# Kernel tuning notes

Hardware: AMD Instinct MI355X
Metric: run time of the kernel (lower is better)

Reference implementation:

```python
import jax, jax.numpy as jnp
import numpy as np

N_NODES = 100000
N_EDGES = 1600000
N_OBS, N_MID, N_ACT = 32, 64, 8


def setup_inputs() -> dict:
    key = jax.random.key(0)
    k1, k2, k3, k4, k5, k6 = jax.random.split(key, 6)
    x = jax.random.normal(k1, (N_NODES, N_OBS), dtype=jnp.float32)
    edge_index = jax.random.randint(k2, (2, N_EDGES), 0, N_NODES, dtype=jnp.int64)
    W1 = jax.random.normal(k3, (N_OBS, N_MID), dtype=jnp.float32) / np.sqrt(N_OBS)
    b1 = jax.random.normal(k4, (N_MID,), dtype=jnp.float32) * 0.01
    W2 = jax.random.normal(k5, (N_MID, N_ACT), dtype=jnp.float32) / np.sqrt(N_MID)
    b2 = jax.random.normal(k6, (N_ACT,), dtype=jnp.float32) * 0.01
    return {"x": x, "edge_index": edge_index, "W1": W1, "b1": b1, "W2": W2, "b2": b2}


def reference(x, edge_index, W1, b1, W2, b2):
    N = x.shape[0]
    # PyG GCNConv: add self-loops, symmetric deg^{-1/2} normalization,
    # linear transform before propagation, bias after aggregation.
    loops = jnp.arange(N, dtype=edge_index.dtype)
    src = jnp.concatenate([edge_index[0], loops])  # message sources (x_j)
    dst = jnp.concatenate([edge_index[1], loops])  # aggregation targets
    deg = jax.ops.segment_sum(jnp.ones_like(dst, dtype=x.dtype), dst, num_segments=N)
    dinv = jnp.where(deg > 0, jax.lax.rsqrt(deg), jnp.zeros_like(deg))
    norm = dinv[src] * dinv[dst]  # [E+N]
    h = x @ W1  # [N, n_mid]
    agg = jax.ops.segment_sum(h[src] * norm[:, None], dst, num_segments=N) + b1
    return jnp.tanh(agg) @ W2 + b2  # [N, n_action]
```

## Files before the change

kernel.cpp:

```cpp
#include <hip/hip_runtime.h>
#include <hip/hip_fp16.h>
#include <math.h>


#define NOBS 32
#define NMID 64
#define NACT 8
#define BSH 7
#define BNODES 128
#define CAP 4096
#define ARENA_B 16384
#define SPLIT_E 4096
#define NPW 4

__device__ __forceinline__ bool edges_i64(const int* ei) {
    return (ei[1] | ei[3] | ei[5] | ei[7]) == 0;
}

__device__ __forceinline__ float fast_tanh(float x) {
    float t = __expf(2.f * x);
    return 1.f - 2.f * __builtin_amdgcn_rcpf(1.f + t);
}

__device__ __forceinline__ float rl(float v, int lane) {
    return __int_as_float(__builtin_amdgcn_readlane(__float_as_int(v), lane));
}

__global__ __launch_bounds__(256) void k_split(
        const int* __restrict__ ei, int* __restrict__ gcnt,
        unsigned int* __restrict__ arena, long long e, int nbuckets) {
    __shared__ int sbuf[SPLIT_E];
    __shared__ int offs[1024];
    __shared__ int cur[1024];
    __shared__ int tsum[256];
    const int tid = threadIdx.x;
    int eb[16];
    int bk[16];

    for (int b = tid; b < 1024; b += 256) cur[b] = 0;
    __syncthreads();

    const long long base = (long long)blockIdx.x * SPLIT_E;
    const bool i64 = edges_i64(ei);
    const long long* e64 = (const long long*)ei;
#pragma unroll
    for (int j = 0; j < 8; ++j) {
        const int kk = j * 512 + tid * 2;
        const long long ge = base + kk;
        const bool v0 = ge < e, v1 = ge + 1 < e;
        int s0 = 0, d0 = 0, s1 = 0, d1 = 0;
        if (v1) {
            if (i64) {
                ulonglong2 sp = *(const ulonglong2*)(e64 + ge);
                ulonglong2 dp = *(const ulonglong2*)(e64 + e + ge);
                s0 = (int)sp.x; s1 = (int)sp.y; d0 = (int)dp.x; d1 = (int)dp.y;
            } else {
                int2 sp = *(const int2*)(ei + ge);
                int2 dp = *(const int2*)(ei + e + ge);
                s0 = sp.x; s1 = sp.y; d0 = dp.x; d1 = dp.y;
            }
        } else if (v0) {
            if (i64) { s0 = (int)e64[ge]; d0 = (int)e64[e + ge]; }
            else     { s0 = ei[ge];       d0 = ei[e + ge]; }
        }
        eb[2 * j]     = s0 | ((d0 & (BNODES - 1)) << 20);
        bk[2 * j]     = v0 ? (d0 >> BSH) : -1;
        eb[2 * j + 1] = s1 | ((d1 & (BNODES - 1)) << 20);
        bk[2 * j + 1] = v1 ? (d1 >> BSH) : -1;
        if (v0) atomicAdd(&cur[d0 >> BSH], 1);
        if (v1) atomicAdd(&cur[d1 >> BSH], 1);
    }
    __syncthreads();

    const int t4 = tid * 4;
    int s0 = cur[t4], s1 = cur[t4 + 1], s2 = cur[t4 + 2], s3 = cur[t4 + 3];
    int my = s0 + s1 + s2 + s3;
    tsum[tid] = my;
    __syncthreads();
    for (int off = 1; off < 256; off <<= 1) {
        int t = (tid >= off) ? tsum[tid - off] : 0;
        __syncthreads();
        tsum[tid] += t;
        __syncthreads();
    }
    int ex = tsum[tid] - my;
    offs[t4] = ex;
    offs[t4 + 1] = ex + s0;
    offs[t4 + 2] = ex + s0 + s1;
    offs[t4 + 3] = ex + s0 + s1 + s2;
    __syncthreads();
    for (int b = tid; b < 1024; b += 256) cur[b] = offs[b];
    __syncthreads();

#pragma unroll
    for (int j = 0; j < 16; ++j) {
        if (bk[j] >= 0) {
            int slot = atomicAdd(&cur[bk[j]], 1);
            sbuf[slot] = eb[j];
        }
    }
    __syncthreads();

    for (int b = tid; b < nbuckets; b += 256) {
        int beg = offs[b];
        int len = cur[b] - beg;
        if (len <= 0) continue;
        int g = atomicAdd(&gcnt[b], len);
        if (g >= CAP) continue;
        if (g + len > CAP) len = CAP - g;
        unsigned int* dst = arena + (size_t)b * CAP + g;
        for (int j = 0; j < len; ++j) dst[j] = (unsigned int)sbuf[beg + j];
    }
}

__global__ __launch_bounds__(256) void k_sort(
        const int* __restrict__ gcnt, unsigned int* __restrict__ arena,
        const float* __restrict__ x, uint2* __restrict__ pkd,
        __half2* __restrict__ y2, int n) {
    __shared__ unsigned int sbuf[CAP];
    __shared__ unsigned int obuf[CAP];
    __shared__ int hist[BNODES];
    __shared__ int offs[BNODES];
    __shared__ int cur[BNODES];
    __shared__ float rinv[BNODES];
    const int b = blockIdx.x, tid = threadIdx.x;
    const int count = min(gcnt[b], CAP);
    unsigned int* ent = arena + (size_t)b * CAP;

    if (tid < BNODES) hist[tid] = 0;
    __syncthreads();
    for (int p = tid; p < count; p += 256) {
        unsigned int v = ent[p];
        sbuf[p] = v;
        atomicAdd(&hist[v >> 20], 1);
    }
    __syncthreads();
    if (tid < BNODES) offs[tid] = hist[tid];
    __syncthreads();
    for (int off = 1; off < BNODES; off <<= 1) {
        int t = 0;
        if (tid < BNODES && tid >= off) t = offs[tid - off];
        __syncthreads();
        if (tid < BNODES) offs[tid] += t;
        __syncthreads();
    }
    if (tid < BNODES) {
        int ex = offs[tid] - hist[tid];
        cur[tid] = ex;
        float r = rsqrtf((float)(hist[tid] + 1));
        rinv[tid] = r;
        int node = b * BNODES + tid;
        if (node < n) {
            uint2 pd;
            pd.x = (unsigned int)(b * CAP + ex) | ((unsigned int)hist[tid] << 22);
            pd.y = __float_as_uint(r);
            pkd[node] = pd;
        }
    }
    __syncthreads();
    for (int p = tid; p < count; p += 256) {
        unsigned int v = sbuf[p];
        int pos = atomicAdd(&cur[v >> 20], 1);
        obuf[pos] = v;
    }
    for (int idx = tid; idx < BNODES * 16; idx += 256) {
        int node = b * BNODES + (idx >> 4);
        if (node >= n) break;
        float r = rinv[idx >> 4];
        float2 v = ((const float2*)x)[(size_t)node * 16 + (idx & 15)];
        y2[(size_t)node * 16 + (idx & 15)] = __floats2half2_rn(v.x * r, v.y * r);
    }
    __syncthreads();
    for (int p = tid; p < count; p += 256) ent[p] = obuf[p];
}

__global__ __launch_bounds__(256, 4) void k_fused(
        const unsigned int* __restrict__ arena, const uint2* __restrict__ pkd,
        const __half2* __restrict__ y2,
        const float* __restrict__ W1, const float* __restrict__ b1,
        const float* __restrict__ W2, const float* __restrict__ b2,
        float* __restrict__ out, int n) {
    __shared__ float sT[4][NMID];
    const int tid = threadIdx.x;
    const int wid = tid >> 6;
    const int lane = tid & 63;
    const int g = lane >> 3, l = lane & 7;
    const int jg = lane >> 3, k = lane & 7;

    float w1col[NOBS];
#pragma unroll
    for (int c = 0; c < NOBS; ++c) w1col[c] = W1[c * NMID + lane];
    float w2row[8];
#pragma unroll
    for (int jj = 0; jj < 8; ++jj) w2row[jj] = W2[(jg * 8 + jj) * NACT + k];
    const float b1v = b1[lane];
    const float b2v = b2[k];

    const int nodeBase = blockIdx.x * (4 * NPW) + wid * NPW;
    const uint2 zero2 = make_uint2(0u, 0u);

    uint2 pd[NPW];
    uint2 sv[NPW];
#pragma unroll
    for (int nn = 0; nn < NPW; ++nn) {
        const int node = nodeBase + nn;
        const bool valid = node < n;
        pd[nn] = valid ? pkd[node] : make_uint2(0u, 0u);
        sv[nn] = (valid && g == 0)
                   ? ((const uint2*)(y2 + (size_t)node * 16))[l] : zero2;
    }
    unsigned int en[4];
    {
        const int beg0 = (int)(pd[0].x & 0x3FFFFF);
#pragma unroll
        for (int w = 0; w < 4; ++w) en[w] = arena[beg0 + g + 8 * w];
    }

#pragma unroll
    for (int nn = 0; nn < NPW; ++nn) {
        const int node = nodeBase + nn;
        const bool valid = node < n;

        const int beg = (int)(pd[nn].x & 0x3FFFFF);
        const int cnt = valid ? (int)(pd[nn].x >> 22) : 0;
        const float din = __uint_as_float(pd[nn].y);

        bool ok[4];
        uint2 v[4];
#pragma unroll
        for (int w = 0; w < 4; ++w) {
            ok[w] = g + 8 * w < cnt;
            const unsigned idx = ok[w] ? (en[w] & 0xFFFFF) : 0u;
            v[w] = ((const uint2*)(y2 + (size_t)idx * 16))[l];
        }

        if (nn + 1 < NPW) {
            const int begN = (int)(pd[nn + 1].x & 0x3FFFFF);
#pragma unroll
            for (int w = 0; w < 4; ++w) en[w] = arena[begN + g + 8 * w];
        }

        float4 acc;
        {
            float2 f0 = __half22float2(*reinterpret_cast<const __half2*>(&sv[nn].x));
            float2 f1 = __half22float2(*reinterpret_cast<const __half2*>(&sv[nn].y));
            acc = make_float4(f0.x, f0.y, f1.x, f1.y);
        }
#pragma unroll
        for (int w = 0; w < 4; ++w) {
            if (!ok[w]) v[w] = zero2;
            float2 a0 = __half22float2(*reinterpret_cast<const __half2*>(&v[w].x));
            float2 a1 = __half22float2(*reinterpret_cast<const __half2*>(&v[w].y));
            acc.x += a0.x; acc.y += a0.y; acc.z += a1.x; acc.w += a1.y;
        }
        if (cnt > 32) {
            for (int i = 32 + g; i < cnt; i += 8) {
                unsigned int ee = arena[beg + i];
                uint2 vv = ((const uint2*)(y2 + (size_t)(ee & 0xFFFFF) * 16))[l];
                float2 a0 = __half22float2(*reinterpret_cast<const __half2*>(&vv.x));
                float2 a1 = __half22float2(*reinterpret_cast<const __half2*>(&vv.y));
                acc.x += a0.x; acc.y += a0.y; acc.z += a1.x; acc.w += a1.y;
            }
        }
#pragma unroll
        for (int off = 8; off < 64; off <<= 1) {
            acc.x += __shfl_xor(acc.x, off); acc.y += __shfl_xor(acc.y, off);
            acc.z += __shfl_xor(acc.z, off); acc.w += __shfl_xor(acc.w, off);
        }
        acc.x *= din; acc.y *= din; acc.z *= din; acc.w *= din;

        float m0 = b1v, m1 = 0.f, m2 = 0.f, m3 = 0.f;
#pragma unroll
        for (int s = 0; s < 8; ++s) {
            m0 = fmaf(rl(acc.x, s), w1col[4 * s + 0], m0);
            m1 = fmaf(rl(acc.y, s), w1col[4 * s + 1], m1);
            m2 = fmaf(rl(acc.z, s), w1col[4 * s + 2], m2);
            m3 = fmaf(rl(acc.w, s), w1col[4 * s + 3], m3);
        }
        sT[wid][lane] = fast_tanh((m0 + m1) + (m2 + m3));
        asm volatile("s_waitcnt lgkmcnt(0)" ::: "memory");
        __builtin_amdgcn_sched_barrier(0);

        float o = 0.f;
#pragma unroll
        for (int jj = 0; jj < 8; ++jj)
            o = fmaf(sT[wid][jg * 8 + jj], w2row[jj], o);
        o += __shfl_xor(o, 8);
        o += __shfl_xor(o, 16);
        o += __shfl_xor(o, 32);
        if (valid && jg == 0)
            out[(size_t)node * NACT + k] = o + b2v;
    }
}

extern "C" void kernel_launch(void* const* d_in, const int* in_sizes, int n_in,
                              void* d_out, int out_size, void* d_ws, size_t ws_size,
                              hipStream_t stream) {
    const float* x  = (const float*)d_in[0];
    const int*   ei = (const int*)d_in[1];
    const float* W1 = (const float*)d_in[2];
    const float* b1 = (const float*)d_in[3];
    const float* W2 = (const float*)d_in[4];
    const float* b2 = (const float*)d_in[5];
    float* out = (float*)d_out;

    const int n = in_sizes[0] / NOBS;
    const long long e = in_sizes[1] / 2;
    const int B = (n + BNODES - 1) >> BSH;

    char* ws = (char*)d_ws;
    int*          gcnt  = (int*)ws;
    unsigned int* arena = (unsigned int*)(ws + 4096);
    uint2*        pkd   = (uint2*)(ws + 4096 + (size_t)B * ARENA_B);
    __half2*      y2    = (__half2*)(ws + 4096 + (size_t)B * ARENA_B + (size_t)n * 8);

    hipMemsetAsync(gcnt, 0, 4096, stream);
    int nsb = (int)((e + SPLIT_E - 1) / SPLIT_E);
    k_split<<<nsb, 256, 0, stream>>>(ei, gcnt, arena, e, B);
    k_sort<<<B, 256, 0, stream>>>(gcnt, arena, x, pkd, y2, n);
    const int npb = 4 * NPW;
    k_fused<<<(n + npb - 1) / npb, 256, 0, stream>>>(arena, pkd, y2,
                                                     W1, b1, W2, b2, out, n);
}
```

Before: 95.98 us.

## Accumulate neighbor sums in packed fp16 and use fdot2 for W1 matvec

Neighbor features are now summed as packed half2 values with packed adds instead of being converted to fp32 and accumulated. W1 is converted to packed half2 registers, and the 32x64 projection uses v_dot2 fp16 instructions with the dinv scale folded into one final fma. Address computation switches to 32-bit unsigned byte offsets. This cuts conversion ALU work and register pressure (16 packed registers instead of 32 floats for W1), at the cost of fp16 accumulation error and overflow risk on high-degree nodes.

Result: faster. 84.07 us (-12.4%).

```diff
diff --git a/kernel.cpp b/kernel.cpp
--- a/kernel.cpp
+++ b/kernel.cpp
@@ -13,6 +13,8 @@
 #define SPLIT_E 4096
 #define NPW 4
 
+typedef _Float16 half2v __attribute__((ext_vector_type(2)));
+
 __device__ __forceinline__ bool edges_i64(const int* ei) {
     return (ei[1] | ei[3] | ei[5] | ei[7]) == 0;
 }
@@ -22,8 +24,19 @@
     return 1.f - 2.f * __builtin_amdgcn_rcpf(1.f + t);
 }
 
-__device__ __forceinline__ float rl(float v, int lane) {
-    return __int_as_float(__builtin_amdgcn_readlane(__float_as_int(v), lane));
+__device__ __forceinline__ unsigned rlu(unsigned v, int lane) {
+    return (unsigned)__builtin_amdgcn_readlane((int)v, lane);
+}
+
+__device__ __forceinline__ unsigned padd(unsigned a, unsigned b) {
+    __half2 r = __hadd2(__builtin_bit_cast(__half2, a),
+                        __builtin_bit_cast(__half2, b));
+    return __builtin_bit_cast(unsigned, r);
+}
+
+__device__ __forceinline__ float fdot2u(unsigned a, unsigned b, float c) {
+    return __builtin_amdgcn_fdot2(__builtin_bit_cast(half2v, a),
+                                  __builtin_bit_cast(half2v, b), c, false);
 }
 
 __global__ __launch_bounds__(256) void k_split(
@@ -186,10 +199,15 @@
     const int lane = tid & 63;
     const int g = lane >> 3, l = lane & 7;
     const int jg = lane >> 3, k = lane & 7;
-
-    float w1col[NOBS];
-#pragma unroll
-    for (int c = 0; c < NOBS; ++c) w1col[c] = W1[c * NMID + lane];
+    const char* y2c = (const char*)y2;
+
+    unsigned w1h[16];
+#pragma unroll
+    for (int c2 = 0; c2 < 16; ++c2) {
+        __half2 h = __floats2half2_rn(W1[(2 * c2) * NMID + lane],
+                                      W1[(2 * c2 + 1) * NMID + lane]);
+        w1h[c2] = __builtin_bit_cast(unsigned, h);
+    }
     float w2row[8];
 #pragma unroll
     for (int jj = 0; jj < 8; ++jj) w2row[jj] = W2[(jg * 8 + jj) * NACT + k];
@@ -197,7 +215,6 @@
     const float b2v = b2[k];
 
     const int nodeBase = blockIdx.x * (4 * NPW) + wid * NPW;
-    const uint2 zero2 = make_uint2(0u, 0u);
 
     uint2 pd[NPW];
     uint2 sv[NPW];
@@ -206,12 +223,15 @@
         const int node = nodeBase + nn;
         const bool valid = node < n;
         pd[nn] = valid ? pkd[node] : make_uint2(0u, 0u);
-        sv[nn] = (valid && g == 0)
-                   ? ((const uint2*)(y2 + (size_t)node * 16))[l] : zero2;
+        sv[nn] = make_uint2(0u, 0u);
+        if (valid && g == 0) {
+            unsigned off = ((unsigned)node << 6) | ((unsigned)l << 3);
+            sv[nn] = *(const uint2*)(y2c + off);
+        }
     }
     unsigned int en[4];
     {
-        const int beg0 = (int)(pd[0].x & 0x3FFFFF);
+        const unsigned beg0 = pd[0].x & 0x3FFFFF;
 #pragma unroll
         for (int w = 0; w < 4; ++w) en[w] = arena[beg0 + g + 8 * w];
     }
@@ -221,7 +241,7 @@
         const int node = nodeBase + nn;
         const bool valid = node < n;
 
-        const int beg = (int)(pd[nn].x & 0x3FFFFF);
+        const unsigned beg = pd[nn].x & 0x3FFFFF;
         const int cnt = valid ? (int)(pd[nn].x >> 22) : 0;
         const float din = __uint_as_float(pd[nn].y);
 
@@ -231,53 +251,46 @@
         for (int w = 0; w < 4; ++w) {
             ok[w] = g + 8 * w < cnt;
             const unsigned idx = ok[w] ? (en[w] & 0xFFFFF) : 0u;
-            v[w] = ((const uint2*)(y2 + (size_t)idx * 16))[l];
+            const unsigned off = (idx << 6) | ((unsigned)l << 3);
+            v[w] = *(const uint2*)(y2c + off);
         }
 
         if (nn + 1 < NPW) {
-            const int begN = (int)(pd[nn + 1].x & 0x3FFFFF);
+            const unsigned begN = pd[nn + 1].x & 0x3FFFFF;
 #pragma unroll
             for (int w = 0; w < 4; ++w) en[w] = arena[begN + g + 8 * w];
         }
 
-        float4 acc;
-        {
-            float2 f0 = __half22float2(*reinterpret_cast<const __half2*>(&sv[nn].x));
-            float2 f1 = __half22float2(*reinterpret_cast<const __half2*>(&sv[nn].y));
-            acc = make_float4(f0.x, f0.y, f1.x, f1.y);
-        }
+        unsigned acc0 = sv[nn].x, acc1 = sv[nn].y;
 #pragma unroll
         for (int w = 0; w < 4; ++w) {
-            if (!ok[w]) v[w] = zero2;
-            float2 a0 = __half22float2(*reinterpret_cast<const __half2*>(&v[w].x));
-            float2 a1 = __half22float2(*reinterpret_cast<const __half2*>(&v[w].y));
-            acc.x += a0.x; acc.y += a0.y; acc.z += a1.x; acc.w += a1.y;
+            if (!ok[w]) { v[w].x = 0u; v[w].y = 0u; }
+            acc0 = padd(acc0, v[w].x);
+            acc1 = padd(acc1, v[w].y);
         }
         if (cnt > 32) {
             for (int i = 32 + g; i < cnt; i += 8) {
-                unsigned int ee = arena[beg + i];
-                uint2 vv = ((const uint2*)(y2 + (size_t)(ee & 0xFFFFF) * 16))[l];
-                float2 a0 = __half22float2(*reinterpret_cast<const __half2*>(&vv.x));
-                float2 a1 = __half22float2(*reinterpret_cast<const __half2*>(&vv.y));
-                acc.x += a0.x; acc.y += a0.y; acc.z += a1.x; acc.w += a1.y;
+                unsigned ee = arena[beg + i];
+                unsigned off = ((ee & 0xFFFFF) << 6) | ((unsigned)l << 3);
+                uint2 vv = *(const uint2*)(y2c + off);
+                acc0 = padd(acc0, vv.x);
+                acc1 = padd(acc1, vv.y);
             }
         }
 #pragma unroll
         for (int off = 8; off < 64; off <<= 1) {
-            acc.x += __shfl_xor(acc.x, off); acc.y += __shfl_xor(acc.y, off);
-            acc.z += __shfl_xor(acc.z, off); acc.w += __shfl_xor(acc.w, off);
-        }
-        acc.x *= din; acc.y *= din; acc.z *= din; acc.w *= din;
-
-        float m0 = b1v, m1 = 0.f, m2 = 0.f, m3 = 0.f;
+            acc0 = padd(acc0, (unsigned)__shfl_xor((int)acc0, off));
+            acc1 = padd(acc1, (unsigned)__shfl_xor((int)acc1, off));
+        }
+
+        float sA = 0.f, sB = 0.f;
 #pragma unroll
         for (int s = 0; s < 8; ++s) {
-            m0 = fmaf(rl(acc.x, s), w1col[4 * s + 0], m0);
-            m1 = fmaf(rl(acc.y, s), w1col[4 * s + 1], m1);
-            m2 = fmaf(rl(acc.z, s), w1col[4 * s + 2], m2);
-            m3 = fmaf(rl(acc.w, s), w1col[4 * s + 3], m3);
-        }
-        sT[wid][lane] = fast_tanh((m0 + m1) + (m2 + m3));
+            sA = fdot2u(rlu(acc0, s), w1h[2 * s + 0], sA);
+            sB = fdot2u(rlu(acc1, s), w1h[2 * s + 1], sB);
+        }
+        const float m = fmaf(din, sA + sB, b1v);
+        sT[wid][lane] = fast_tanh(m);
         asm volatile("s_waitcnt lgkmcnt(0)" ::: "memory");
         __builtin_amdgcn_sched_barrier(0);
 
```
